# Performance work log

Measured on AMD Instinct MI355X. Metric: run time of the kernel, lower is better.

## Reference

```python
import jax, jax.numpy as jnp
import numpy as np

N, E, NC, F0, MID = 20000, 320000, 16, 67, 32
Y0 = 0.28209479177387814   # 1/(2*sqrt(pi)), real spherical harmonic l=0
C1 = 0.4886025119029199    # sqrt(3/(4*pi)),  real spherical harmonic l=1 coeff


def setup_inputs() -> dict:
    key = jax.random.key(0)
    ks = jax.random.split(key, 16)
    rn = lambda k, shape, s=1.0: jax.random.normal(k, shape, dtype=jnp.float32) * s
    return {
        "node_feats": rn(ks[0], (N, F0)),
        "pos": rn(ks[1], (N, 3)) * 3.0,
        "edge_w": jax.random.uniform(ks[2], (E, 2), dtype=jnp.float32),
        "lin1_W": rn(ks[5], (F0, F0), 1.0 / np.sqrt(F0)),
        "lin1_b": jnp.zeros((F0,), jnp.float32),
        "lin2_W": rn(ks[6], (F0, NC), 1.0 / np.sqrt(F0)),
        "lin2_b": jnp.zeros((NC,), jnp.float32),
        # 4 radial nets = 2 GConv layers x 2 degree pairs ((0,0),(0,1))
        "rW1": rn(ks[7], (4, 3, MID), 1.0 / np.sqrt(3)),
        "rb1": jnp.zeros((4, MID), jnp.float32),
        "ln1_g": jnp.ones((4, MID), jnp.float32),
        "ln1_b": jnp.zeros((4, MID), jnp.float32),
        "rW2": rn(ks[8], (4, MID, MID), 1.0 / np.sqrt(MID)),
        "rb2": jnp.zeros((4, MID), jnp.float32),
        "ln2_g": jnp.ones((4, MID), jnp.float32),
        "ln2_b": jnp.zeros((4, MID), jnp.float32),
        "rW3": rn(ks[9], (4, MID, NC * NC), 1.0 / np.sqrt(MID)),
        "rb3": jnp.zeros((4, NC * NC), jnp.float32),
        "Wself": rn(ks[10], (2, NC, NC), 1.0 / np.sqrt(NC)),
        "src": jax.random.randint(ks[3], (E,), 0, N),
        "dst": jax.random.randint(ks[4], (E,), 0, N),
    }


def _layer_norm(x, g, b, eps=1e-5):
    mu = jnp.mean(x, -1, keepdims=True)
    var = jnp.mean((x - mu) ** 2, -1, keepdims=True)
    return (x - mu) * jax.lax.rsqrt(var + eps) * g + b


def _forward(node_feats, pos, edge_w, lin1_W, lin1_b, lin2_W, lin2_b,
             rW1, rb1, ln1_g, ln1_b, rW2, rb2, ln2_g, ln2_b, rW3, rb3,
             Wself, src, dst):
    # node embedding: Linear -> ELU -> (dropout p=0) -> Linear -> [N, NC]
    h0 = jax.nn.elu(node_feats @ lin1_W + lin1_b) @ lin2_W + lin2_b

    # get_basis_and_r: relative positions, radial distance, SH basis (d_in=0)
    d = pos[dst] - pos[src]                                   # [E, 3]
    r = jnp.sqrt(jnp.sum(d * d, -1))                          # [E]
    rhat = d / jnp.maximum(r, 1e-8)[:, None]
    Y1 = C1 * rhat[:, jnp.array([1, 2, 0])]                   # [E, 3] (y, z, x order)
    feat = jnp.concatenate([edge_w, r[:, None]], -1)          # [E, edge_dim+1=3]

    deg = jax.ops.segment_sum(jnp.ones((E,), feat.dtype), dst, num_segments=N)
    inv_deg = jnp.where(deg > 0, 1.0 / jnp.maximum(deg, 1.0), 0.0)
    has_in = (deg > 0).astype(feat.dtype)

    def radial(i):
        h = jnp.maximum(_layer_norm(feat @ rW1[i] + rb1[i], ln1_g[i], ln1_b[i]), 0.0)
        h = jnp.maximum(_layer_norm(h @ rW2[i] + rb2[i], ln2_g[i], ln2_b[i]), 0.0)
        return (h @ rW3[i] + rb3[i]).reshape(E, NC, NC)       # [E, nc_out, nc_in]

    out1 = None
    for li in range(2):  # faithful to source bug: both layers read only degree-0 feats
        R00 = radial(2 * li)        # pairwise kernel (0->0), num_freq=1
        R01 = radial(2 * li + 1)    # pairwise kernel (0->1), num_freq=1
        s = h0[src]                                           # [E, NC] gather
        msg0 = Y0 * jnp.einsum('eoi,ei->eo', R00, s)          # [E, NC]
        msg1 = jnp.einsum('eoi,ei,em->eom', R01, s, Y1)       # [E, NC, 3]
        out0 = jax.ops.segment_sum(msg0, dst, num_segments=N) * inv_deg[:, None]
        out0 = out0 + has_in[:, None] * (h0 @ Wself[li].T)    # self-interaction (deg 0)
        out1 = jax.ops.segment_sum(msg1, dst, num_segments=N) * inv_deg[:, None, None]
        h0 = out0
    return h0[:, :, None], out1                               # {'0': [N,NC,1], '1': [N,NC,3]}


def reference(node_feats, pos, edge_w, lin1_W, lin1_b, lin2_W, lin2_b,
              rW1, rb1, ln1_g, ln1_b, rW2, rb2, ln2_g, ln2_b, rW3, rb3,
              Wself, src, dst):
    return _forward(node_feats, pos, edge_w, lin1_W, lin1_b, lin2_W, lin2_b,
                    rW1, rb1, ln1_g, ln1_b, rW2, rb2, ln2_g, ln2_b, rW3, rb3,
                    Wself, src, dst)
```

## Files before the change

### kernel.cpp

```cpp
#include <hip/hip_runtime.h>
#include <hip/hip_fp16.h>


#define Y0C 0.28209479177387814f
#define C1C 0.4886025119029199f

typedef _Float16 hv2 __attribute__((ext_vector_type(2)));

#if defined(__has_builtin)
#if __has_builtin(__builtin_amdgcn_fdot2)
#define FDOT2(a, b, c) __builtin_amdgcn_fdot2((a), (b), (c), false)
#endif
#endif
#ifndef FDOT2
#define FDOT2(a, b, c) ((c) + (float)(a).x * (float)(b).x + (float)(a).y * (float)(b).y)
#endif

static __device__ __forceinline__ unsigned h2u(__half2 h) {
    union { __half2 h; unsigned u; } x; x.h = h; return x.u;
}
static __device__ __forceinline__ __half2 u2h(unsigned u) {
    union { unsigned u; __half2 h; } x; x.u = u; return x.h;
}
static __device__ __forceinline__ hv2 u2hv(unsigned u) {
    union { unsigned u; hv2 h; } x; x.u = u; return x.h;
}
static __device__ __forceinline__ unsigned hv2u(hv2 h) {
    union { hv2 h; unsigned u; } x; x.h = h; return x.u;
}
static __device__ __forceinline__ hv2 f2hv(float a, float b) {
    hv2 r; r.x = (_Float16)a; r.y = (_Float16)b; return r;
}
static __device__ __forceinline__ float hbits2f(unsigned short s) {
    __half_raw r; r.x = s; return __half2float((__half)r);
}

struct RadialW {
    const float *W1, *b1, *g1, *gb1, *b2, *g2, *gb2;
    const unsigned* W2q;
};

__device__ __forceinline__ void radial_net_pk(float x0, float x1, float x2,
                                              RadialW rw, hv2* hvpk ) {
    float h[32];
#pragma unroll
    for (int j = 0; j < 32; ++j)
        h[j] = rw.b1[j] + x0 * rw.W1[j] + x1 * rw.W1[32 + j] + x2 * rw.W1[64 + j];
    float s0 = 0.f, s1 = 0.f, s2 = 0.f, s3 = 0.f;
#pragma unroll
    for (int p = 0; p < 8; ++p) {
        s0 += h[4 * p]; s1 += h[4 * p + 1]; s2 += h[4 * p + 2]; s3 += h[4 * p + 3];
    }
    float mu = ((s0 + s1) + (s2 + s3)) * 0.03125f;
    float v0 = 0.f, v1 = 0.f, v2 = 0.f, v3 = 0.f;
#pragma unroll
    for (int p = 0; p < 8; ++p) {
        float d0 = h[4 * p] - mu, d1 = h[4 * p + 1] - mu;
        float d2 = h[4 * p + 2] - mu, d3 = h[4 * p + 3] - mu;
        v0 = fmaf(d0, d0, v0); v1 = fmaf(d1, d1, v1);
        v2 = fmaf(d2, d2, v2); v3 = fmaf(d3, d3, v3);
    }
    float var = ((v0 + v1) + (v2 + v3)) * 0.03125f;
    float rs = rsqrtf(var + 1e-5f);
#pragma unroll
    for (int j = 0; j < 32; ++j)
        h[j] = fmaxf((h[j] - mu) * rs * rw.g1[j] + rw.gb1[j], 0.f);

    hv2 hp[16];
#pragma unroll
    for (int p = 0; p < 16; ++p) hp[p] = f2hv(h[2 * p], h[2 * p + 1]);

    float h2[32];
#pragma unroll
    for (int j = 0; j < 32; ++j) {
        float acc = rw.b2[j];
        const unsigned* __restrict__ wj = rw.W2q + j * 16;
#pragma unroll
        for (int kp = 0; kp < 16; ++kp)
            acc = FDOT2(hp[kp], u2hv(wj[kp]), acc);
        h2[j] = acc;
    }
    s0 = s1 = s2 = s3 = 0.f;
#pragma unroll
    for (int p = 0; p < 8; ++p) {
        s0 += h2[4 * p]; s1 += h2[4 * p + 1]; s2 += h2[4 * p + 2]; s3 += h2[4 * p + 3];
    }
    mu = ((s0 + s1) + (s2 + s3)) * 0.03125f;
    v0 = v1 = v2 = v3 = 0.f;
#pragma unroll
    for (int p = 0; p < 8; ++p) {
        float d0 = h2[4 * p] - mu, d1 = h2[4 * p + 1] - mu;
        float d2 = h2[4 * p + 2] - mu, d3 = h2[4 * p + 3] - mu;
        v0 = fmaf(d0, d0, v0); v1 = fmaf(d1, d1, v1);
        v2 = fmaf(d2, d2, v2); v3 = fmaf(d3, d3, v3);
    }
    var = ((v0 + v1) + (v2 + v3)) * 0.03125f;
    rs = rsqrtf(var + 1e-5f);
    float y[32];
#pragma unroll
    for (int j = 0; j < 32; ++j)
        y[j] = fmaxf((h2[j] - mu) * rs * rw.g2[j] + rw.gb2[j], 0.f);
#pragma unroll
    for (int p = 0; p < 16; ++p) hvpk[p] = f2hv(y[2 * p], y[2 * p + 1]);
}

__device__ __forceinline__ void contract_dot(const hv2* hvpk,
                                             const uint4* __restrict__ Um,
                                             const float* __restrict__ Ut,
                                             float* v ) {
    float4 t0 = ((const float4*)Ut)[0];
    float4 t1 = ((const float4*)Ut)[1];
    float4 t2 = ((const float4*)Ut)[2];
    float4 t3 = ((const float4*)Ut)[3];
    float tail[16] = {t0.x, t0.y, t0.z, t0.w, t1.x, t1.y, t1.z, t1.w,
                      t2.x, t2.y, t2.z, t2.w, t3.x, t3.y, t3.z, t3.w};
#pragma unroll
    for (int o = 0; o < 16; ++o) {
        uint4 q0 = Um[o * 4];
        uint4 q1 = Um[o * 4 + 1];
        uint4 q2 = Um[o * 4 + 2];
        uint4 q3 = Um[o * 4 + 3];
        float acc = tail[o];
        acc = FDOT2(hvpk[0],  u2hv(q0.x), acc);
        acc = FDOT2(hvpk[1],  u2hv(q0.y), acc);
        acc = FDOT2(hvpk[2],  u2hv(q0.z), acc);
        acc = FDOT2(hvpk[3],  u2hv(q0.w), acc);
        acc = FDOT2(hvpk[4],  u2hv(q1.x), acc);
        acc = FDOT2(hvpk[5],  u2hv(q1.y), acc);
        acc = FDOT2(hvpk[6],  u2hv(q1.z), acc);
        acc = FDOT2(hvpk[7],  u2hv(q1.w), acc);
        acc = FDOT2(hvpk[8],  u2hv(q2.x), acc);
        acc = FDOT2(hvpk[9],  u2hv(q2.y), acc);
        acc = FDOT2(hvpk[10], u2hv(q2.z), acc);
        acc = FDOT2(hvpk[11], u2hv(q2.w), acc);
        acc = FDOT2(hvpk[12], u2hv(q3.x), acc);
        acc = FDOT2(hvpk[13], u2hv(q3.y), acc);
        acc = FDOT2(hvpk[14], u2hv(q3.z), acc);
        acc = FDOT2(hvpk[15], u2hv(q3.w), acc);
        v[o] = acc;
    }
}

__global__ __launch_bounds__(256) void k_fuse1(
    const float* __restrict__ nf, const float* __restrict__ W1,
    const float* __restrict__ b1, float* __restrict__ t, int N, int nbEmb,
    const float* __restrict__ rW3, const float* __restrict__ rW2,
    unsigned* __restrict__ Wp, unsigned* __restrict__ Wq,
    const int* __restrict__ src, const int* __restrict__ dst,
    int* __restrict__ cntd, int* __restrict__ cnts,
    int* __restrict__ posd, int* __restrict__ poss, int E) {
    if (blockIdx.x >= (unsigned)(nbEmb + 9)) {
        int e = (blockIdx.x - nbEmb - 9) * 256 + threadIdx.x;
        if (e >= E) return;
        posd[e] = atomicAdd(cntd + dst[e], 1);
        poss[e] = atomicAdd(cnts + src[e], 1);
        return;
    }
    if (blockIdx.x >= (unsigned)nbEmb) {
        int tt = (blockIdx.x - nbEmb) * 256 + threadIdx.x;
        if (tt < 3 * 256) {
            int ni = tt >> 8;
            int net = (ni == 0) ? 0 : ni + 1;
            int r = tt & 255;
            int i = r >> 4, o = r & 15;
            const float* __restrict__ W3n = rW3 + (size_t)net * 8192;
            unsigned* __restrict__ dp = Wp + (size_t)ni * 4608 + (size_t)(i * 16 + o) * 18;
#pragma unroll
            for (int kp = 0; kp < 16; ++kp) {
                float a = W3n[(2 * kp) * 256 + o * 16 + i];
                float b = W3n[(2 * kp + 1) * 256 + o * 16 + i];
                dp[kp] = h2u(__floats2half2_rn(a, b));
            }
        } else if (tt < 3 * 256 + 3 * 512) {
            int r = tt - 3 * 256;
            int ni = r / 512;
            int net = (ni == 0) ? 0 : ni + 1;
            int jk = r - ni * 512;
            int j = jk >> 4, kp = jk & 15;
            const float* __restrict__ W2n = rW2 + (size_t)net * 1024;
            Wq[ni * 512 + j * 16 + kp] =
                h2u(__floats2half2_rn(W2n[(2 * kp) * 32 + j],
                                      W2n[(2 * kp + 1) * 32 + j]));
        }
        return;
    }
    int idx = blockIdx.x * 256 + threadIdx.x;
    if (idx >= N * 67) return;
    int n = idx / 67, j = idx - n * 67;
    const float* __restrict__ x = nf + (size_t)n * 67;
    const float* __restrict__ w = W1 + j;
    float a0 = b1[j], a1 = 0.f, a2 = 0.f, a3 = 0.f;
#pragma unroll
    for (int i = 0; i < 64; i += 4) {
        a0 = fmaf(x[i],     w[(size_t)i * 67],       a0);
        a1 = fmaf(x[i + 1], w[(size_t)(i + 1) * 67], a1);
        a2 = fmaf(x[i + 2], w[(size_t)(i + 2) * 67], a2);
        a3 = fmaf(x[i + 3], w[(size_t)(i + 3) * 67], a3);
    }
    a0 = fmaf(x[64], w[64 * 67], a0);
    a1 = fmaf(x[65], w[65 * 67], a1);
    a2 = fmaf(x[66], w[66 * 67], a2);
    float s = (a0 + a1) + (a2 + a3);
    t[idx] = (s > 0.f) ? s : expm1f(s);
}

__global__ __launch_bounds__(1024) void k_fuse2(
    const int* __restrict__ cntd, int* __restrict__ rsd,
    const int* __restrict__ cnts, int* __restrict__ rss, int N,
    const float* __restrict__ t, const float* __restrict__ W2,
    const float* __restrict__ b2, float* __restrict__ h0) {
    if (blockIdx.x < 2) {
        const int* __restrict__ c = (blockIdx.x == 0) ? cntd : cnts;
        int* __restrict__ rs      = (blockIdx.x == 0) ? rsd  : rss;
        int chunk = (N + 1023) >> 10;
        int lo = (int)threadIdx.x * chunk;
        int sum = 0;
        for (int j = 0; j < chunk; ++j) { int i = lo + j; sum += (i < N) ? c[i] : 0; }
        __shared__ int ps[1024];
        ps[threadIdx.x] = sum;
        __syncthreads();
        for (int off = 1; off < 1024; off <<= 1) {
            int v = (threadIdx.x >= (unsigned)off) ? ps[threadIdx.x - off] : 0;
            __syncthreads();
            ps[threadIdx.x] += v;
            __syncthreads();
        }
        int run = threadIdx.x ? ps[threadIdx.x - 1] : 0;
        if (threadIdx.x == 0) rs[0] = 0;
        for (int j = 0; j < chunk; ++j) {
            int i = lo + j;
            if (i < N) { run += c[i]; rs[i + 1] = run; }
        }
        return;
    }
    int idx = (blockIdx.x - 2) * 1024 + threadIdx.x;
    if (idx >= N * 16) return;
    int n = idx >> 4, c = idx & 15;
    const float* __restrict__ x = t + (size_t)n * 67;
    const float* __restrict__ w = W2 + c;
    float a0 = b2[c], a1 = 0.f, a2 = 0.f, a3 = 0.f;
#pragma unroll
    for (int i = 0; i < 64; i += 4) {
        a0 = fmaf(x[i],     w[(size_t)i * 16],       a0);
        a1 = fmaf(x[i + 1], w[(size_t)(i + 1) * 16], a1);
        a2 = fmaf(x[i + 2], w[(size_t)(i + 2) * 16], a2);
        a3 = fmaf(x[i + 3], w[(size_t)(i + 3) * 16], a3);
    }
    a0 = fmaf(x[64], w[64 * 16], a0);
    a1 = fmaf(x[65], w[65 * 16], a1);
    a2 = fmaf(x[66], w[66 * 16], a2);
    h0[idx] = (a0 + a1) + (a2 + a3);
}

__device__ __forceinline__ void u2_body(
    unsigned* WL, int nbase, const float* __restrict__ h,
    const float* __restrict__ b3, unsigned* __restrict__ Um,
    float* __restrict__ Ut, int N) {
    int o = threadIdx.x & 15;
    int pr = threadIdx.x >> 4;
    int n0 = nbase + pr * 2;
    int n1 = n0 + 1;
    bool ok0 = n0 < N, ok1 = n1 < N;
    int m0 = ok0 ? n0 : 0, m1 = ok1 ? n1 : 0;

    const float* __restrict__ bo = b3 + o * 16;
    float tA = 0.f, tB = 0.f;
    __half2 hhA[16], hhB[16];
    {
        const float4* hp = (const float4*)(h + (size_t)m0 * 16);
#pragma unroll
        for (int q = 0; q < 4; ++q) {
            float4 hv = hp[q];
            tA += hv.x * bo[4 * q] + hv.y * bo[4 * q + 1]
                + hv.z * bo[4 * q + 2] + hv.w * bo[4 * q + 3];
            hhA[4 * q]     = __floats2half2_rn(hv.x, hv.x);
            hhA[4 * q + 1] = __floats2half2_rn(hv.y, hv.y);
            hhA[4 * q + 2] = __floats2half2_rn(hv.z, hv.z);
            hhA[4 * q + 3] = __floats2half2_rn(hv.w, hv.w);
        }
    }
    {
        const float4* hp = (const float4*)(h + (size_t)m1 * 16);
#pragma unroll
        for (int q = 0; q < 4; ++q) {
            float4 hv = hp[q];
            tB += hv.x * bo[4 * q] + hv.y * bo[4 * q + 1]
                + hv.z * bo[4 * q + 2] + hv.w * bo[4 * q + 3];
            hhB[4 * q]     = __floats2half2_rn(hv.x, hv.x);
            hhB[4 * q + 1] = __floats2half2_rn(hv.y, hv.y);
            hhB[4 * q + 2] = __floats2half2_rn(hv.z, hv.z);
            hhB[4 * q + 3] = __floats2half2_rn(hv.w, hv.w);
        }
    }

    __half2 accA[16], accB[16];
#pragma unroll
    for (int p = 0; p < 16; ++p) {
        accA[p] = __floats2half2_rn(0.f, 0.f);
        accB[p] = __floats2half2_rn(0.f, 0.f);
    }

#pragma unroll
    for (int i = 0; i < 16; ++i) {
        const uint2* __restrict__ row = (const uint2*)(WL + i * 288 + o * 18);
        __half2 ha = hhA[i], hb = hhB[i];
#pragma unroll
        for (int q = 0; q < 8; ++q) {
            uint2 w = row[q];
            accA[2 * q]     = __hfma2(ha, u2h(w.x), accA[2 * q]);
            accA[2 * q + 1] = __hfma2(ha, u2h(w.y), accA[2 * q + 1]);
            accB[2 * q]     = __hfma2(hb, u2h(w.x), accB[2 * q]);
            accB[2 * q + 1] = __hfma2(hb, u2h(w.y), accB[2 * q + 1]);
        }
    }

    if (ok0) {
        uint4* du = (uint4*)(Um + ((size_t)(n0 * 16 + o)) * 16);
#pragma unroll
        for (int q = 0; q < 4; ++q)
            du[q] = make_uint4(h2u(accA[4 * q]), h2u(accA[4 * q + 1]),
                               h2u(accA[4 * q + 2]), h2u(accA[4 * q + 3]));
        Ut[n0 * 16 + o] = tA;
    }
    if (ok1) {
        uint4* du = (uint4*)(Um + ((size_t)(n1 * 16 + o)) * 16);
#pragma unroll
        for (int q = 0; q < 4; ++q)
            du[q] = make_uint4(h2u(accB[4 * q]), h2u(accB[4 * q + 1]),
                               h2u(accB[4 * q + 2]), h2u(accB[4 * q + 3]));
        Ut[n1 * 16 + o] = tB;
    }
}

__global__ __launch_bounds__(256) void k_fuse3(
    const float* __restrict__ h, const unsigned* __restrict__ Wp,
    const float* __restrict__ b3, unsigned* __restrict__ Um,
    float* __restrict__ Ut, int nbU, int N,
    const float* __restrict__ pos, const float* __restrict__ ew,
    const int* __restrict__ src, const int* __restrict__ dst,
    const int* __restrict__ rsd, const int* __restrict__ rss,
    const int* __restrict__ posd, const int* __restrict__ poss,
    float4* __restrict__ edgeS, uint2* __restrict__ y1d,
    int* __restrict__ s2d, int E) {
    __shared__ unsigned WL[4608];
    if (blockIdx.x < (unsigned)nbU) {
        for (int j = threadIdx.x; j < 4608; j += 256) WL[j] = Wp[j];
        __syncthreads();
        u2_body(WL, blockIdx.x * 32, h, b3, Um, Ut, N);
        return;
    }
    int e = (blockIdx.x - nbU) * 256 + threadIdx.x;
    if (e >= E) return;
    int s = src[e], d = dst[e];
    float dx = pos[3 * d]     - pos[3 * s];
    float dy = pos[3 * d + 1] - pos[3 * s + 1];
    float dz = pos[3 * d + 2] - pos[3 * s + 2];
    float r = sqrtf(dx * dx + dy * dy + dz * dz);
    float im = 1.f / fmaxf(r, 1e-8f);
    int ts = rss[s] + poss[e];
    int td = rsd[d] + posd[e];
    s2d[ts] = td;
    edgeS[ts] = make_float4(ew[2 * e], ew[2 * e + 1], r, __int_as_float(s));
    y1d[td] = make_uint2(h2u(__floats2half2_rn(C1C * dy * im, C1C * dz * im)),
                         h2u(__floats2half2_rn(C1C * dx * im, 0.f)));
}

__global__ __launch_bounds__(256) void k_u2(
    const float* __restrict__ h, const unsigned* __restrict__ Wp,
    const float* __restrict__ b3A, const float* __restrict__ b3B,
    unsigned* __restrict__ Um0, float* __restrict__ Ut0,
    unsigned* __restrict__ Um1, float* __restrict__ Ut1,
    int wpA, int nbPerNet, int N) {
    __shared__ unsigned WL[4608];
    int netSel = blockIdx.x / nbPerNet;
    int nbase = (blockIdx.x - netSel * nbPerNet) * 32;
    const unsigned* __restrict__ g = Wp + (size_t)(wpA + netSel) * 4608;
    for (int j = threadIdx.x; j < 4608; j += 256) WL[j] = g[j];
    __syncthreads();
    u2_body(WL, nbase, h, netSel ? b3B : b3A,
            netSel ? Um1 : Um0, netSel ? Ut1 : Ut0, N);
}

__global__ __launch_bounds__(256) void k_edgeL0(
    const float4* __restrict__ edgeS, const int* __restrict__ s2d, RadialW ra,
    const uint4* __restrict__ UmA, const float* __restrict__ UtA,
    unsigned short* __restrict__ msg , int E) {
    int t = blockIdx.x * blockDim.x + threadIdx.x;
    if (t >= E) return;
    float4 a = edgeS[t];
    int sn = __float_as_int(a.w);
    hv2 hv[16];
    float v[16];
    radial_net_pk(a.x, a.y, a.z, ra, hv);
    contract_dot(hv, UmA + (size_t)sn * 64, UtA + (size_t)sn * 16, v);
    int td = s2d[t];
    uint4* m = (uint4*)(msg + (size_t)td * 16);
    m[0] = make_uint4(hv2u(f2hv(v[0], v[1])),  hv2u(f2hv(v[2], v[3])),
                      hv2u(f2hv(v[4], v[5])),  hv2u(f2hv(v[6], v[7])));
    m[1] = make_uint4(hv2u(f2hv(v[8], v[9])),  hv2u(f2hv(v[10], v[11])),
                      hv2u(f2hv(v[12], v[13])), hv2u(f2hv(v[14], v[15])));
}

__global__ __launch_bounds__(256) void k_edgeL1(
    const float4* __restrict__ edgeS, const int* __restrict__ s2d,
    RadialW ra, RadialW rb,
    const uint4* __restrict__ UmA, const float* __restrict__ UtA,
    const uint4* __restrict__ UmB, const float* __restrict__ UtB,
    unsigned short* __restrict__ msg , int nbE, int E) {
    int half = (blockIdx.x >= (unsigned)nbE) ? 1 : 0;
    int t = (blockIdx.x - half * nbE) * blockDim.x + threadIdx.x;
    if (t >= E) return;
    float4 a = edgeS[t];
    int sn = __float_as_int(a.w);
    RadialW rw = half ? rb : ra;
    const uint4* __restrict__ Um = half ? UmB : UmA;
    const float* __restrict__ Ut = half ? UtB : UtA;
    hv2 hv[16];
    float v[16];
    radial_net_pk(a.x, a.y, a.z, rw, hv);
    contract_dot(hv, Um + (size_t)sn * 64, Ut + (size_t)sn * 16, v);
    int td = s2d[t];
    uint4* m = (uint4*)(msg + (size_t)td * 32 + half * 16);
    m[0] = make_uint4(hv2u(f2hv(v[0], v[1])),  hv2u(f2hv(v[2], v[3])),
                      hv2u(f2hv(v[4], v[5])),  hv2u(f2hv(v[6], v[7])));
    m[1] = make_uint4(hv2u(f2hv(v[8], v[9])),  hv2u(f2hv(v[10], v[11])),
                      hv2u(f2hv(v[12], v[13])), hv2u(f2hv(v[14], v[15])));
}

__global__ void k_reduce0(const unsigned short* __restrict__ msg,
                          const int* __restrict__ rowstart,
                          const float* __restrict__ h, const float* __restrict__ Wself,
                          float* __restrict__ out, int N) {
    int idx = blockIdx.x * blockDim.x + threadIdx.x;
    if (idx >= N * 16) return;
    int n = idx >> 4, o = idx & 15;
    int s = rowstart[n], t1 = rowstart[n + 1];
    float acc0 = 0.f, acc1 = 0.f;
    int t = s;
    for (; t + 1 < t1; t += 2) {
        acc0 += hbits2f(msg[(size_t)t * 16 + o]);
        acc1 += hbits2f(msg[(size_t)(t + 1) * 16 + o]);
    }
    if (t < t1) acc0 += hbits2f(msg[(size_t)t * 16 + o]);
    float acc = acc0 + acc1;
    int d = t1 - s;
    float invd = (d > 0) ? 1.f / (float)d : 0.f;
    float hi   = (d > 0) ? 1.f : 0.f;
    const float* __restrict__ hn = h + (size_t)n * 16;
    const float* __restrict__ w  = Wself + o * 16;
    float self = 0.f;
#pragma unroll
    for (int c = 0; c < 16; ++c) self += hn[c] * w[c];
    out[idx] = Y0C * acc * invd + hi * self;
}

__global__ void k_reduce1(const unsigned short* __restrict__ msg,
                          const uint2* __restrict__ y1d,
                          const int* __restrict__ rowstart,
                          const float* __restrict__ h, const float* __restrict__ Wself,
                          float* __restrict__ out0, float* __restrict__ out1, int N) {
    int idx = blockIdx.x * blockDim.x + threadIdx.x;
    if (idx >= N * 16) return;
    int n = idx >> 4, o = idx & 15;
    int s = rowstart[n], t1 = rowstart[n + 1];
    float a0 = 0.f, ax = 0.f, ay = 0.f, az = 0.f;
    float b0 = 0.f, bx = 0.f, by = 0.f, bz = 0.f;
    int t = s;
    for (; t + 1 < t1; t += 2) {
        const unsigned short* rowA = msg + (size_t)t * 32;
        const unsigned short* rowB = msg + (size_t)(t + 1) * 32;
        uint2 yva = y1d[t];
        uint2 yvb = y1d[t + 1];
        a0 += hbits2f(rowA[o]);
        b0 += hbits2f(rowB[o]);
        float pa = hbits2f(rowA[16 + o]);
        float pb = hbits2f(rowB[16 + o]);
        ax = fmaf(pa, hbits2f((unsigned short)yva.x), ax);
        ay = fmaf(pa, hbits2f((unsigned short)(yva.x >> 16)), ay);
        az = fmaf(pa, hbits2f((unsigned short)yva.y), az);
        bx = fmaf(pb, hbits2f((unsigned short)yvb.x), bx);
        by = fmaf(pb, hbits2f((unsigned short)(yvb.x >> 16)), by);
        bz = fmaf(pb, hbits2f((unsigned short)yvb.y), bz);
    }
    if (t < t1) {
        const unsigned short* rowA = msg + (size_t)t * 32;
        uint2 yva = y1d[t];
        a0 += hbits2f(rowA[o]);
        float pa = hbits2f(rowA[16 + o]);
        ax = fmaf(pa, hbits2f((unsigned short)yva.x), ax);
        ay = fmaf(pa, hbits2f((unsigned short)(yva.x >> 16)), ay);
        az = fmaf(pa, hbits2f((unsigned short)yva.y), az);
    }
    a0 += b0; ax += bx; ay += by; az += bz;
    int d = t1 - s;
    float invd = (d > 0) ? 1.f / (float)d : 0.f;
    float hi   = (d > 0) ? 1.f : 0.f;
    const float* __restrict__ hn = h + (size_t)n * 16;
    const float* __restrict__ w  = Wself + o * 16;
    float self = 0.f;
#pragma unroll
    for (int c = 0; c < 16; ++c) self += hn[c] * w[c];
    out0[idx] = Y0C * a0 * invd + hi * self;
    out1[(size_t)idx * 3]     = ax * invd;
    out1[(size_t)idx * 3 + 1] = ay * invd;
    out1[(size_t)idx * 3 + 2] = az * invd;
}

extern "C" void kernel_launch(void* const* d_in, const int* in_sizes, int n_in,
                              void* d_out, int out_size, void* d_ws, size_t ws_size,
                              hipStream_t stream) {
    (void)n_in; (void)out_size; (void)ws_size;
    const float* node_feats = (const float*)d_in[0];
    const float* pos    = (const float*)d_in[1];
    const float* edge_w = (const float*)d_in[2];
    const float* lin1_W = (const float*)d_in[3];
    const float* lin1_b = (const float*)d_in[4];
    const float* lin2_W = (const float*)d_in[5];
    const float* lin2_b = (const float*)d_in[6];
    const float* rW1    = (const float*)d_in[7];
    const float* rb1    = (const float*)d_in[8];
    const float* ln1_g  = (const float*)d_in[9];
    const float* ln1_b  = (const float*)d_in[10];
    const float* rW2    = (const float*)d_in[11];
    const float* rb2    = (const float*)d_in[12];
    const float* ln2_g  = (const float*)d_in[13];
    const float* ln2_b  = (const float*)d_in[14];
    const float* rW3    = (const float*)d_in[15];
    const float* rb3    = (const float*)d_in[16];
    const float* Wself  = (const float*)d_in[17];
    const int*   src    = (const int*)d_in[18];
    const int*   dst    = (const int*)d_in[19];

    const int N = in_sizes[1] / 3;
    const int E = in_sizes[18];

    char* ws = (char*)d_ws;
    size_t off = 0;
    auto carve = [&](size_t bytes) -> char* {
        char* p = ws + off;
        off = (off + bytes + 255) & ~(size_t)255;
        return p;
    };
    float* h0   = (float*)carve((size_t)N * 16 * 4);
    float* h1   = (float*)carve((size_t)N * 16 * 4);
    int*   cntd = (int*)carve((size_t)N * 4);
    int*   cnts = (int*)carve((size_t)N * 4);
    int*   rsd  = (int*)carve((size_t)(N + 1) * 4);
    int*   rss  = (int*)carve((size_t)(N + 1) * 4);
    int*   s2d  = (int*)carve((size_t)E * 4);
    float4* edgeS = (float4*)carve((size_t)E * 16);
    uint2*  y1d   = (uint2*)carve((size_t)E * 8);
    unsigned* UaM = (unsigned*)carve((size_t)N * 16 * 64);
    float*    UaT = (float*)carve((size_t)N * 16 * 4);
    unsigned* UbM = (unsigned*)carve((size_t)N * 16 * 64);
    float*    UbT = (float*)carve((size_t)N * 16 * 4);
    unsigned* Wp  = (unsigned*)carve((size_t)3 * 4608 * 4);
    unsigned* Wq  = (unsigned*)carve((size_t)3 * 512 * 4);
    unsigned short* msg = (unsigned short*)carve((size_t)E * 32 * 2);
    float* tmb = (float*)msg;
    int* posd = (int*)((char*)msg + (8u << 20));
    int* poss = (int*)((char*)msg + (14u << 20));

    auto nb = [](int n) { return (n + 255) / 256; };
    const int nbE = nb(E);
    const int nbU = (N + 31) / 32;
    const int nbE1 = nb(N * 67);

    hipMemsetAsync(cntd, 0, (size_t)((char*)cnts - (char*)cntd) + (size_t)N * 4, stream);

    k_fuse1<<<nbE1 + 9 + nbE, 256, 0, stream>>>(node_feats, lin1_W, lin1_b, tmb, N,
                                                nbE1, rW3, rW2, Wp, Wq,
                                                src, dst, cntd, cnts, posd, poss, E);
    k_fuse2<<<2 + (N * 16 + 1023) / 1024, 1024, 0, stream>>>(
        cntd, rsd, cnts, rss, N, tmb, lin2_W, lin2_b, h0);
    k_fuse3<<<nbU + nbE, 256, 0, stream>>>(h0, Wp, rb3, UaM, UaT, nbU, N,
                                           pos, edge_w, src, dst, rsd, rss,
                                           posd, poss, edgeS, y1d, s2d, E);

    auto rnet = [&](int net, int ni) -> RadialW {
        RadialW r;
        r.W1 = rW1 + net * 96;   r.b1 = rb1 + net * 32;
        r.g1 = ln1_g + net * 32; r.gb1 = ln1_b + net * 32;
        r.b2 = rb2 + net * 32;
        r.g2 = ln2_g + net * 32; r.gb2 = ln2_b + net * 32;
        r.W2q = Wq + ni * 512;
        return r;
    };

    k_edgeL0<<<nbE, 256, 0, stream>>>(edgeS, s2d, rnet(0, 0), (const uint4*)UaM, UaT,
                                      msg, E);
    k_reduce0<<<nb(N * 16), 256, 0, stream>>>(msg, rsd, h0, Wself, h1, N);

    k_u2<<<2 * nbU, 256, 0, stream>>>(h1, Wp, rb3 + 2 * 256, rb3 + 3 * 256,
                                      UaM, UaT, UbM, UbT, 1, nbU, N);
    k_edgeL1<<<2 * nbE, 256, 0, stream>>>(edgeS, s2d, rnet(2, 1), rnet(3, 2),
                                          (const uint4*)UaM, UaT,
                                          (const uint4*)UbM, UbT, msg, nbE, E);
    float* out0 = (float*)d_out;
    float* out1 = (float*)d_out + (size_t)N * 16;
    k_reduce1<<<nb(N * 16), 256, 0, stream>>>(msg, y1d, rsd, h1, Wself + 256,
                                              out0, out1, N);
}
```

Baseline: 328.2 us.

## Replace global atomic edge ranking with blocked LDS histogram counting sort

The per-edge global atomicAdd used to compute counts and within-bucket positions for dst and src is replaced by a three-pass scheme. Each of 128 blocks per key builds a packed 16-bit shared-memory histogram, a partition kernel turns these into per-block exclusive offsets and totals, and a final pass recomputes local ranks with shared atomics. This removes heavy global atomic contention and the memset, and makes edge ordering deterministic. In exchange it adds two kernel launches and about 10 MB of histogram traffic. It also relies on N fitting in 40 KB of LDS and on per-block counts fitting in 16 bits.

```diff
diff --git a/kernel.cpp b/kernel.cpp
--- a/kernel.cpp
+++ b/kernel.cpp
@@ -4,6 +4,7 @@
 
 #define Y0C 0.28209479177387814f
 #define C1C 0.4886025119029199f
+#define CSB 128
 
 typedef _Float16 hv2 __attribute__((ext_vector_type(2)));
 
@@ -141,21 +142,74 @@
     }
 }
 
+__global__ __launch_bounds__(256) void k_histA(
+    const int* __restrict__ srcA, const int* __restrict__ dstA,
+    unsigned short* __restrict__ histD, unsigned short* __restrict__ histS,
+    int N, int E, int EB) {
+    __shared__ unsigned h32[10240];
+    int r = (blockIdx.x >= (unsigned)CSB) ? 1 : 0;
+    int b = blockIdx.x - r * CSB;
+    const int* __restrict__ key = r ? srcA : dstA;
+    unsigned short* __restrict__ out = (r ? histS : histD) + (size_t)b * N;
+    int half = (N + 1) >> 1;
+    for (int i = threadIdx.x; i < half; i += 256) h32[i] = 0;
+    __syncthreads();
+    int lo = b * EB, hi = min(E, lo + EB);
+    for (int e = lo + (int)threadIdx.x; e < hi; e += 256) {
+        int k = key[e];
+        atomicAdd(&h32[k >> 1], 1u << ((k & 1) * 16));
+    }
+    __syncthreads();
+    for (int n = threadIdx.x; n < N; n += 256)
+        out[n] = (unsigned short)((h32[n >> 1] >> ((n & 1) * 16)) & 0xffffu);
+}
+
+__global__ __launch_bounds__(256) void k_partB(
+    unsigned short* __restrict__ histD, unsigned short* __restrict__ histS,
+    int* __restrict__ totD, int* __restrict__ totS, int N) {
+    int idx = blockIdx.x * 256 + threadIdx.x;
+    if (idx >= 2 * N) return;
+    int r = (idx >= N) ? 1 : 0;
+    int n = idx - r * N;
+    unsigned short* __restrict__ hist = r ? histS : histD;
+    int run = 0;
+#pragma unroll 4
+    for (int b = 0; b < CSB; ++b) {
+        size_t o = (size_t)b * N + n;
+        int t = hist[o];
+        hist[o] = (unsigned short)run;
+        run += t;
+    }
+    (r ? totS : totD)[n] = run;
+}
+
+__global__ __launch_bounds__(256) void k_posC(
+    const int* __restrict__ srcA, const int* __restrict__ dstA,
+    const unsigned short* __restrict__ histD, const unsigned short* __restrict__ histS,
+    int* __restrict__ posd, int* __restrict__ poss, int N, int E, int EB) {
+    __shared__ unsigned h32[10240];
+    int r = (blockIdx.x >= (unsigned)CSB) ? 1 : 0;
+    int b = blockIdx.x - r * CSB;
+    const int* __restrict__ key = r ? srcA : dstA;
+    const unsigned short* __restrict__ part = (r ? histS : histD) + (size_t)b * N;
+    int* __restrict__ pos = r ? poss : posd;
+    int half = (N + 1) >> 1;
+    for (int i = threadIdx.x; i < half; i += 256) h32[i] = 0;
+    __syncthreads();
+    int lo = b * EB, hi = min(E, lo + EB);
+    for (int e = lo + (int)threadIdx.x; e < hi; e += 256) {
+        int k = key[e];
+        unsigned old = atomicAdd(&h32[k >> 1], 1u << ((k & 1) * 16));
+        int lrank = (int)((old >> ((k & 1) * 16)) & 0xffffu);
+        pos[e] = (int)part[k] + lrank;
+    }
+}
+
 __global__ __launch_bounds__(256) void k_fuse1(
     const float* __restrict__ nf, const float* __restrict__ W1,
     const float* __restrict__ b1, float* __restrict__ t, int N, int nbEmb,
     const float* __restrict__ rW3, const float* __restrict__ rW2,
-    unsigned* __restrict__ Wp, unsigned* __restrict__ Wq,
-    const int* __restrict__ src, const int* __restrict__ dst,
-    int* __restrict__ cntd, int* __restrict__ cnts,
-    int* __restrict__ posd, int* __restrict__ poss, int E) {
-    if (blockIdx.x >= (unsigned)(nbEmb + 9)) {
-        int e = (blockIdx.x - nbEmb - 9) * 256 + threadIdx.x;
-        if (e >= E) return;
-        posd[e] = atomicAdd(cntd + dst[e], 1);
-        poss[e] = atomicAdd(cnts + src[e], 1);
-        return;
-    }
+    unsigned* __restrict__ Wp, unsigned* __restrict__ Wq) {
     if (blockIdx.x >= (unsigned)nbEmb) {
         int tt = (blockIdx.x - nbEmb) * 256 + threadIdx.x;
         if (tt < 3 * 256) {
@@ -168,8 +222,8 @@
 #pragma unroll
             for (int kp = 0; kp < 16; ++kp) {
                 float a = W3n[(2 * kp) * 256 + o * 16 + i];
-                float b = W3n[(2 * kp + 1) * 256 + o * 16 + i];
-                dp[kp] = h2u(__floats2half2_rn(a, b));
+                float b2v = W3n[(2 * kp + 1) * 256 + o * 16 + i];
+                dp[kp] = h2u(__floats2half2_rn(a, b2v));
             }
         } else if (tt < 3 * 256 + 3 * 512) {
             int r = tt - 3 * 256;
@@ -205,12 +259,12 @@
 }
 
 __global__ __launch_bounds__(1024) void k_fuse2(
-    const int* __restrict__ cntd, int* __restrict__ rsd,
-    const int* __restrict__ cnts, int* __restrict__ rss, int N,
+    const int* __restrict__ totD, int* __restrict__ rsd,
+    const int* __restrict__ totS, int* __restrict__ rss, int N,
     const float* __restrict__ t, const float* __restrict__ W2,
     const float* __restrict__ b2, float* __restrict__ h0) {
     if (blockIdx.x < 2) {
-        const int* __restrict__ c = (blockIdx.x == 0) ? cntd : cnts;
+        const int* __restrict__ c = (blockIdx.x == 0) ? totD : totS;
         int* __restrict__ rs      = (blockIdx.x == 0) ? rsd  : rss;
         int chunk = (N + 1023) >> 10;
         int lo = (int)threadIdx.x * chunk;
@@ -543,8 +597,10 @@
     };
     float* h0   = (float*)carve((size_t)N * 16 * 4);
     float* h1   = (float*)carve((size_t)N * 16 * 4);
-    int*   cntd = (int*)carve((size_t)N * 4);
-    int*   cnts = (int*)carve((size_t)N * 4);
+    unsigned short* histD = (unsigned short*)carve((size_t)CSB * N * 2);
+    unsigned short* histS = (unsigned short*)carve((size_t)CSB * N * 2);
+    int*   totD = (int*)carve((size_t)N * 4);
+    int*   totS = (int*)carve((size_t)N * 4);
     int*   rsd  = (int*)carve((size_t)(N + 1) * 4);
     int*   rss  = (int*)carve((size_t)(N + 1) * 4);
     int*   s2d  = (int*)carve((size_t)E * 4);
@@ -565,14 +621,16 @@
     const int nbE = nb(E);
     const int nbU = (N + 31) / 32;
     const int nbE1 = nb(N * 67);
-
-    hipMemsetAsync(cntd, 0, (size_t)((char*)cnts - (char*)cntd) + (size_t)N * 4, stream);
-
-    k_fuse1<<<nbE1 + 9 + nbE, 256, 0, stream>>>(node_feats, lin1_W, lin1_b, tmb, N,
-                                                nbE1, rW3, rW2, Wp, Wq,
-                                                src, dst, cntd, cnts, posd, poss, E);
+    const int EB = (E + CSB - 1) / CSB;
+
+    k_histA<<<2 * CSB, 256, 0, stream>>>(src, dst, histD, histS, N, E, EB);
+    k_fuse1<<<nbE1 + 9, 256, 0, stream>>>(node_feats, lin1_W, lin1_b, tmb, N,
+                                          nbE1, rW3, rW2, Wp, Wq);
+    k_partB<<<nb(2 * N), 256, 0, stream>>>(histD, histS, totD, totS, N);
     k_fuse2<<<2 + (N * 16 + 1023) / 1024, 1024, 0, stream>>>(
-        cntd, rsd, cnts, rss, N, tmb, lin2_W, lin2_b, h0);
+        totD, rsd, totS, rss, N, tmb, lin2_W, lin2_b, h0);
+    k_posC<<<2 * CSB, 256, 0, stream>>>(src, dst, histD, histS, posd, poss,
+                                        N, E, EB);
     k_fuse3<<<nbU + nbE, 256, 0, stream>>>(h0, Wp, rb3, UaM, UaT, nbU, N,
                                            pos, edge_w, src, dst, rsd, rss,
                                            posd, poss, edgeS, y1d, s2d, E);
```

Result: slower. 340.7 us (+3.8%).

## Fuse layer-0 reduction with layer-1 per-node U precompute into one kernel

Applied to the files above, without the earlier changes.

Merges k_reduce0 and k_u2 into a single kernel. Each 256-thread block reduces messages for 16 nodes, keeps the resulting h1 rows in shared memory, and immediately computes the per-node U matrices for both radial nets from them. This saves one launch and the global round trip of h1 into the U kernel. In exchange every block (16 nodes instead of 32 per net) loads 36 KB of weights into shared memory, which raises per-block weight-load traffic and LDS use and may lower occupancy.

```diff
diff --git a/kernel.cpp b/kernel.cpp
--- a/kernel.cpp
+++ b/kernel.cpp
@@ -365,20 +365,104 @@
                          h2u(__floats2half2_rn(C1C * dx * im, 0.f)));
 }
 
-__global__ __launch_bounds__(256) void k_u2(
-    const float* __restrict__ h, const unsigned* __restrict__ Wp,
-    const float* __restrict__ b3A, const float* __restrict__ b3B,
-    unsigned* __restrict__ Um0, float* __restrict__ Ut0,
-    unsigned* __restrict__ Um1, float* __restrict__ Ut1,
-    int wpA, int nbPerNet, int N) {
-    __shared__ unsigned WL[4608];
-    int netSel = blockIdx.x / nbPerNet;
-    int nbase = (blockIdx.x - netSel * nbPerNet) * 32;
-    const unsigned* __restrict__ g = Wp + (size_t)(wpA + netSel) * 4608;
-    for (int j = threadIdx.x; j < 4608; j += 256) WL[j] = g[j];
+__global__ __launch_bounds__(256) void k_redu(
+    const unsigned short* __restrict__ msg, const int* __restrict__ rsd,
+    const float* __restrict__ h0, const float* __restrict__ Wself,
+    const unsigned* __restrict__ Wp, const float* __restrict__ rb3,
+    float* __restrict__ h1,
+    unsigned* __restrict__ UaM, float* __restrict__ UaT,
+    unsigned* __restrict__ UbM, float* __restrict__ UbT, int N) {
+    __shared__ unsigned WL[9216];
+    __shared__ float h1L[16][17];
+    for (int j = threadIdx.x; j < 9216; j += 256) WL[j] = Wp[4608 + j];
+
+    int ln = threadIdx.x >> 4, o = threadIdx.x & 15;
+    int n = blockIdx.x * 16 + ln;
+    float val = 0.f;
+    if (n < N) {
+        int s = rsd[n], t1 = rsd[n + 1];
+        float acc0 = 0.f, acc1 = 0.f;
+        int t = s;
+        for (; t + 1 < t1; t += 2) {
+            acc0 += hbits2f(msg[(size_t)t * 16 + o]);
+            acc1 += hbits2f(msg[(size_t)(t + 1) * 16 + o]);
+        }
+        if (t < t1) acc0 += hbits2f(msg[(size_t)t * 16 + o]);
+        float acc = acc0 + acc1;
+        int d = t1 - s;
+        float invd = (d > 0) ? 1.f / (float)d : 0.f;
+        float hi   = (d > 0) ? 1.f : 0.f;
+        const float* __restrict__ hn = h0 + (size_t)n * 16;
+        const float* __restrict__ w  = Wself + o * 16;
+        float self = 0.f;
+#pragma unroll
+        for (int c = 0; c < 16; ++c) self += hn[c] * w[c];
+        val = Y0C * acc * invd + hi * self;
+        h1[(size_t)n * 16 + o] = val;
+    }
+    h1L[ln][o] = val;
     __syncthreads();
-    u2_body(WL, nbase, h, netSel ? b3B : b3A,
-            netSel ? Um1 : Um0, netSel ? Ut1 : Ut0, N);
+
+    int net = threadIdx.x >> 7;
+    int rem = threadIdx.x & 127;
+    int p = rem >> 4, oo = rem & 15;
+    int n0 = blockIdx.x * 16 + 2 * p;
+    int n1 = n0 + 1;
+    bool ok0 = n0 < N, ok1 = n1 < N;
+    const float* __restrict__ b3 = rb3 + (net ? 3 : 2) * 256;
+    unsigned* __restrict__ Um = net ? UbM : UaM;
+    float*    __restrict__ Ut = net ? UbT : UaT;
+    const float* __restrict__ bo = b3 + oo * 16;
+
+    float tA = 0.f, tB = 0.f;
+    __half2 hhA[16], hhB[16];
+#pragma unroll
+    for (int i = 0; i < 16; ++i) {
+        float a = h1L[2 * p][i];
+        float b = h1L[2 * p + 1][i];
+        float bv = bo[i];
+        tA = fmaf(a, bv, tA);
+        tB = fmaf(b, bv, tB);
+        hhA[i] = __floats2half2_rn(a, a);
+        hhB[i] = __floats2half2_rn(b, b);
+    }
+
+    __half2 accA[16], accB[16];
+#pragma unroll
+    for (int q = 0; q < 16; ++q) {
+        accA[q] = __floats2half2_rn(0.f, 0.f);
+        accB[q] = __floats2half2_rn(0.f, 0.f);
+    }
+    const unsigned* __restrict__ WLn = WL + net * 4608;
+#pragma unroll
+    for (int i = 0; i < 16; ++i) {
+        const uint2* __restrict__ row = (const uint2*)(WLn + i * 288 + oo * 18);
+        __half2 ha = hhA[i], hb = hhB[i];
+#pragma unroll
+        for (int q = 0; q < 8; ++q) {
+            uint2 w = row[q];
+            accA[2 * q]     = __hfma2(ha, u2h(w.x), accA[2 * q]);
+            accA[2 * q + 1] = __hfma2(ha, u2h(w.y), accA[2 * q + 1]);
+            accB[2 * q]     = __hfma2(hb, u2h(w.x), accB[2 * q]);
+            accB[2 * q + 1] = __hfma2(hb, u2h(w.y), accB[2 * q + 1]);
+        }
+    }
+    if (ok0) {
+        uint4* du = (uint4*)(Um + ((size_t)(n0 * 16 + oo)) * 16);
+#pragma unroll
+        for (int q = 0; q < 4; ++q)
+            du[q] = make_uint4(h2u(accA[4 * q]), h2u(accA[4 * q + 1]),
+                               h2u(accA[4 * q + 2]), h2u(accA[4 * q + 3]));
+        Ut[n0 * 16 + oo] = tA;
+    }
+    if (ok1) {
+        uint4* du = (uint4*)(Um + ((size_t)(n1 * 16 + oo)) * 16);
+#pragma unroll
+        for (int q = 0; q < 4; ++q)
+            du[q] = make_uint4(h2u(accB[4 * q]), h2u(accB[4 * q + 1]),
+                               h2u(accB[4 * q + 2]), h2u(accB[4 * q + 3]));
+        Ut[n1 * 16 + oo] = tB;
+    }
 }
 
 __global__ __launch_bounds__(256) void k_edgeL0(
@@ -425,33 +509,6 @@
                       hv2u(f2hv(v[4], v[5])),  hv2u(f2hv(v[6], v[7])));
     m[1] = make_uint4(hv2u(f2hv(v[8], v[9])),  hv2u(f2hv(v[10], v[11])),
                       hv2u(f2hv(v[12], v[13])), hv2u(f2hv(v[14], v[15])));
-}
-
-__global__ void k_reduce0(const unsigned short* __restrict__ msg,
-                          const int* __restrict__ rowstart,
-                          const float* __restrict__ h, const float* __restrict__ Wself,
-                          float* __restrict__ out, int N) {
-    int idx = blockIdx.x * blockDim.x + threadIdx.x;
-    if (idx >= N * 16) return;
-    int n = idx >> 4, o = idx & 15;
-    int s = rowstart[n], t1 = rowstart[n + 1];
-    float acc0 = 0.f, acc1 = 0.f;
-    int t = s;
-    for (; t + 1 < t1; t += 2) {
-        acc0 += hbits2f(msg[(size_t)t * 16 + o]);
-        acc1 += hbits2f(msg[(size_t)(t + 1) * 16 + o]);
-    }
-    if (t < t1) acc0 += hbits2f(msg[(size_t)t * 16 + o]);
-    float acc = acc0 + acc1;
-    int d = t1 - s;
-    float invd = (d > 0) ? 1.f / (float)d : 0.f;
-    float hi   = (d > 0) ? 1.f : 0.f;
-    const float* __restrict__ hn = h + (size_t)n * 16;
-    const float* __restrict__ w  = Wself + o * 16;
-    float self = 0.f;
-#pragma unroll
-    for (int c = 0; c < 16; ++c) self += hn[c] * w[c];
-    out[idx] = Y0C * acc * invd + hi * self;
 }
 
 __global__ void k_reduce1(const unsigned short* __restrict__ msg,
@@ -565,6 +622,7 @@
     const int nbE = nb(E);
     const int nbU = (N + 31) / 32;
     const int nbE1 = nb(N * 67);
+    const int nbR = (N + 15) / 16;
 
     hipMemsetAsync(cntd, 0, (size_t)((char*)cnts - (char*)cntd) + (size_t)N * 4, stream);
 
@@ -589,10 +647,8 @@
 
     k_edgeL0<<<nbE, 256, 0, stream>>>(edgeS, s2d, rnet(0, 0), (const uint4*)UaM, UaT,
                                       msg, E);
-    k_reduce0<<<nb(N * 16), 256, 0, stream>>>(msg, rsd, h0, Wself, h1, N);
-
-    k_u2<<<2 * nbU, 256, 0, stream>>>(h1, Wp, rb3 + 2 * 256, rb3 + 3 * 256,
-                                      UaM, UaT, UbM, UbT, 1, nbU, N);
+    k_redu<<<nbR, 256, 0, stream>>>(msg, rsd, h0, Wself, Wp, rb3, h1,
+                                    UaM, UaT, UbM, UbT, N);
     k_edgeL1<<<2 * nbE, 256, 0, stream>>>(edgeS, s2d, rnet(2, 1), rnet(3, 2),
                                           (const uint4*)UaM, UaT,
                                           (const uint4*)UbM, UbT, msg, nbE, E);
```

Result: slower. 339.4 us (+3.4%).
